# Optimization experiments

Measured on AMD Instinct MI355X. Metric: run time of the kernel, lower is better.

Reference implementation:

```python
import jax, jax.numpy as jnp
import numpy as np

# SMPL-H kintree parents for the first 22 joints (kintree_table[0][:22]); root parent is unused.
SMPL_PARENT = np.array([0, 0, 0, 0, 1, 2, 3, 4, 5, 6, 7, 8, 9, 9, 9, 12, 13, 14, 16, 17, 18, 19], dtype=np.int64)

EPS = 1e-12


def _sixd2matrot(d6):
    # d6: [..., 6] -> R: [..., 3, 3] (rows b1,b2,b3), pytorch3d rotation_6d_to_matrix convention
    a1, a2 = d6[..., :3], d6[..., 3:]
    b1 = a1 / jnp.maximum(jnp.linalg.norm(a1, axis=-1, keepdims=True), EPS)
    a2p = a2 - jnp.sum(b1 * a2, axis=-1, keepdims=True) * b1
    b2 = a2p / jnp.maximum(jnp.linalg.norm(a2p, axis=-1, keepdims=True), EPS)
    b3 = jnp.cross(b1, b2)
    return jnp.stack([b1, b2, b3], axis=-2)


def setup_inputs() -> dict:
    key = jax.random.key(0)
    B, T, J = 512, 196, 22
    pred_pose = jax.random.normal(key, (B, T, J * 6), dtype=jnp.float32)
    return {"pred_pose": pred_pose, "parent": SMPL_PARENT}


def reference(pred_pose, parent):
    B, T, C = pred_pose.shape  # C = 22*6
    J = C // 6
    parent = np.asarray(parent)  # static tree structure
    d6 = pred_pose.reshape(B * T, J, 6)
    R_local = _sixd2matrot(d6)  # [N, J, 3, 3]
    # forward kinematics along the tree: R_global[i] = R_global[parent[i]] @ R_local[i]
    R_global = [R_local[:, 0]]
    for i in range(1, J):
        R_global.append(jnp.einsum('nij,njk->nik', R_global[int(parent[i])], R_local[:, i]))
    R_global = jnp.stack(R_global, axis=1)  # [N, J, 3, 3]
    # matrot -> 6d: first two rows flattened
    rotation_global_r6d = R_global[..., :2, :].reshape(B, T, J * 6)
    return rotation_global_r6d
```

## Files before the change

kernel.cpp:

```cpp
#include <hip/hip_runtime.h>


#define TPB 256

namespace {
constexpr int PAR1[22] = {0,0,0,0,1,2,3,4,5,6,7,8,9,9,9,12,13,14,16,17,18,19};
constexpr int PAR2[22] = {0,0,0,0,0,0,0,1,2,3,4,5,6,6,6,9,9,9,13,14,16,17};
constexpr int PAR4[22] = {0,0,0,0,0,0,0,0,0,0,0,0,0,0,0,3,3,3,6,6,9,9};

__device__ __host__ constexpr unsigned long long pack5(const int (&t)[22], int base) {
    unsigned long long v = 0;
    for (int i = 0; i < 11; ++i)
        v |= (unsigned long long)(t[base + i] & 31) << (5 * i);
    return v;
}
constexpr unsigned long long P1L = pack5(PAR1, 0), P1H = pack5(PAR1, 11);
constexpr unsigned long long P2L = pack5(PAR2, 0), P2H = pack5(PAR2, 11);
constexpr unsigned long long P4L = pack5(PAR4, 0), P4H = pack5(PAR4, 11);
}

__device__ __forceinline__ void mm3(float* __restrict__ D, const float* __restrict__ P,
                                    const float* __restrict__ L) {
#pragma unroll
    for (int r = 0; r < 3; ++r)
#pragma unroll
        for (int c = 0; c < 3; ++c)
            D[3 * r + c] = P[3 * r + 0] * L[0 + c] +
                           P[3 * r + 1] * L[3 + c] +
                           P[3 * r + 2] * L[6 + c];
}

__global__ __launch_bounds__(TPB) void fk6d_kernel(const float* __restrict__ in,
                                                   float* __restrict__ out, int N)
{
    const int tid = threadIdx.x;
    const int lane = tid & 63;
    const int base = lane & 32;
    const int j = lane & 31;
    const int frame = blockIdx.x * 8 + ((tid >> 6) << 1) + (lane >> 5);
    const bool act = (j < 22) && (frame < N);
    const int jc = (j < 22) ? j : 21;
    const int jm = (jc < 11) ? jc : jc - 11;
    const int sh = 5 * jm;

    const int a1 = (int)(((jc < 11) ? P1L : P1H) >> sh) & 31;
    const int a2 = (int)(((jc < 11) ? P2L : P2H) >> sh) & 31;
    const int a4 = (int)(((jc < 11) ? P4L : P4H) >> sh) & 31;

    float A[9];
    if (act) {
        const float* s = in + (size_t)frame * 132 + j * 6;
        float2 d0 = *reinterpret_cast<const float2*>(s);
        float2 d1 = *reinterpret_cast<const float2*>(s + 2);
        float2 d2 = *reinterpret_cast<const float2*>(s + 4);
        float a1x = d0.x, a1y = d0.y, a1z = d1.x;
        float a2x = d1.y, a2y = d2.x, a2z = d2.y;
        float n1 = sqrtf(a1x * a1x + a1y * a1y + a1z * a1z);
        float i1 = 1.0f / fmaxf(n1, 1e-12f);
        float b1x = a1x * i1, b1y = a1y * i1, b1z = a1z * i1;
        float dt = b1x * a2x + b1y * a2y + b1z * a2z;
        float cx = a2x - dt * b1x, cy = a2y - dt * b1y, cz = a2z - dt * b1z;
        float n2 = sqrtf(cx * cx + cy * cy + cz * cz);
        float i2 = 1.0f / fmaxf(n2, 1e-12f);
        A[0] = b1x; A[1] = b1y; A[2] = b1z;
        A[3] = cx * i2; A[4] = cy * i2; A[5] = cz * i2;
        A[6] = A[1] * A[5] - A[2] * A[4];
        A[7] = A[2] * A[3] - A[0] * A[5];
        A[8] = A[0] * A[4] - A[1] * A[3];
    } else {
#pragma unroll
        for (int k = 0; k < 9; ++k) A[k] = 0.0f;
    }

    {
        float M[9], T[9];
        int src = base | a1;
#pragma unroll
        for (int k = 0; k < 9; ++k) M[k] = __shfl(A[k], src, 64);
        mm3(T, M, A);
        bool on = (j >= 1);
#pragma unroll
        for (int k = 0; k < 9; ++k) A[k] = on ? T[k] : A[k];
    }
    {
        float M[9], T[9];
        int src = base | a2;
#pragma unroll
        for (int k = 0; k < 9; ++k) M[k] = __shfl(A[k], src, 64);
        mm3(T, M, A);
        bool on = (j >= 4);
#pragma unroll
        for (int k = 0; k < 9; ++k) A[k] = on ? T[k] : A[k];
    }
    {
        float M[9], T[9];
        int src = base | a4;
#pragma unroll
        for (int k = 0; k < 9; ++k) M[k] = __shfl(A[k], src, 64);
        mm3(T, M, A);
        bool on = (j >= 10);
#pragma unroll
        for (int k = 0; k < 9; ++k) A[k] = on ? T[k] : A[k];
    }

    if (act) {
        float* d = out + (size_t)frame * 132 + j * 6;
        *reinterpret_cast<float2*>(d)     = make_float2(A[0], A[1]);
        *reinterpret_cast<float2*>(d + 2) = make_float2(A[2], A[3]);
        *reinterpret_cast<float2*>(d + 4) = make_float2(A[4], A[5]);
    }
}

extern "C" void kernel_launch(void* const* d_in, const int* in_sizes, int n_in,
                              void* d_out, int out_size, void* d_ws, size_t ws_size,
                              hipStream_t stream) {
    const float* in = (const float*)d_in[0];
    float* out = (float*)d_out;
    int N = in_sizes[0] / 132;
    int grid = (N + 7) / 8;
    fk6d_kernel<<<grid, TPB, 0, stream>>>(in, out, N);
}
```

Baseline: 28.75 us.

## Stage frame tiles through LDS with async global-to-LDS loads and coalesced stores

Each block now handles a 16-frame tile. The tile is loaded straight into shared memory with global_load_lds, which replaces the strided float2 global loads. Results are written back into LDS, then copied out to global memory as contiguous float4 stores. Block size doubles to 512 with a launch-bounds occupancy hint. A scalar tail kernel covers leftover frames, and it adds a barrier and LDS pressure per block.

```diff
diff --git a/kernel.cpp b/kernel.cpp
--- a/kernel.cpp
+++ b/kernel.cpp
@@ -1,7 +1,9 @@
 #include <hip/hip_runtime.h>
 
 
-#define TPB 256
+#define TPB 512
+#define TILE_FRAMES 16
+#define TILE_FLOATS (TILE_FRAMES * 132)
 
 namespace {
 constexpr int PAR1[22] = {0,0,0,0,1,2,3,4,5,6,7,8,9,9,9,12,13,14,16,17,18,19};
@@ -30,26 +32,43 @@
                            P[3 * r + 2] * L[6 + c];
 }
 
-__global__ __launch_bounds__(TPB) void fk6d_kernel(const float* __restrict__ in,
-                                                   float* __restrict__ out, int N)
+__global__ __launch_bounds__(TPB, 6) void fk6d_kernel(const float* __restrict__ in,
+                                                      float* __restrict__ out)
 {
+    __shared__ float lds[TILE_FLOATS];
     const int tid = threadIdx.x;
+    const int wid = tid >> 6;
     const int lane = tid & 63;
+
+    const float* gin = in + (size_t)blockIdx.x * TILE_FLOATS;
+    float* gout = out + (size_t)blockIdx.x * TILE_FLOATS;
+
+    __builtin_amdgcn_global_load_lds(
+        (const __attribute__((address_space(1))) void*)(gin + wid * 256 + lane * 4),
+        (__attribute__((address_space(3))) void*)(lds + wid * 256), 16, 0, 0);
+    if (wid == 0) {
+        __builtin_amdgcn_global_load_lds(
+            (const __attribute__((address_space(1))) void*)(gin + 2048 + lane),
+            (__attribute__((address_space(3))) void*)(lds + 2048), 4, 0, 0);
+    }
+    __syncthreads();
+
     const int base = lane & 32;
     const int j = lane & 31;
-    const int frame = blockIdx.x * 8 + ((tid >> 6) << 1) + (lane >> 5);
-    const bool act = (j < 22) && (frame < N);
-    const int jc = (j < 22) ? j : 21;
+    const int frame = wid * 2 + (lane >> 5);
+    const bool act = (j < 22);
+    const int jc = act ? j : 21;
     const int jm = (jc < 11) ? jc : jc - 11;
     const int sh = 5 * jm;
-
     const int a1 = (int)(((jc < 11) ? P1L : P1H) >> sh) & 31;
     const int a2 = (int)(((jc < 11) ? P2L : P2H) >> sh) & 31;
     const int a4 = (int)(((jc < 11) ? P4L : P4H) >> sh) & 31;
 
     float A[9];
+#pragma unroll
+    for (int k = 0; k < 9; ++k) A[k] = 0.0f;
     if (act) {
-        const float* s = in + (size_t)frame * 132 + j * 6;
+        const float* s = lds + frame * 132 + j * 6;
         float2 d0 = *reinterpret_cast<const float2*>(s);
         float2 d1 = *reinterpret_cast<const float2*>(s + 2);
         float2 d2 = *reinterpret_cast<const float2*>(s + 4);
@@ -67,9 +86,6 @@
         A[6] = A[1] * A[5] - A[2] * A[4];
         A[7] = A[2] * A[3] - A[0] * A[5];
         A[8] = A[0] * A[4] - A[1] * A[3];
-    } else {
-#pragma unroll
-        for (int k = 0; k < 9; ++k) A[k] = 0.0f;
     }
 
     {
@@ -104,10 +120,52 @@
     }
 
     if (act) {
-        float* d = out + (size_t)frame * 132 + j * 6;
+        float* d = lds + frame * 132 + j * 6;
         *reinterpret_cast<float2*>(d)     = make_float2(A[0], A[1]);
         *reinterpret_cast<float2*>(d + 2) = make_float2(A[2], A[3]);
         *reinterpret_cast<float2*>(d + 4) = make_float2(A[4], A[5]);
+    }
+    __syncthreads();
+
+    const float4* l4 = reinterpret_cast<const float4*>(lds);
+    float4* o4 = reinterpret_cast<float4*>(gout);
+#pragma unroll
+    for (int t = tid; t < TILE_FLOATS / 4; t += TPB) o4[t] = l4[t];
+}
+
+__global__ void fk6d_tail(const float* __restrict__ in, float* __restrict__ out,
+                          int n0, int N) {
+    constexpr int PAR[22] = {0, 0, 0, 0, 1, 2, 3, 4, 5, 6, 7, 8, 9, 9, 9,
+                             12, 13, 14, 16, 17, 18, 19};
+    int n = n0 + blockIdx.x * blockDim.x + threadIdx.x;
+    if (n >= N) return;
+    const float* src = in + (size_t)n * 132;
+    float* dst = out + (size_t)n * 132;
+    float Rg[22][9];
+#pragma unroll
+    for (int j = 0; j < 22; ++j) {
+        const float* s = src + 6 * j;
+        float Lr[9];
+        float n1 = sqrtf(s[0]*s[0] + s[1]*s[1] + s[2]*s[2]);
+        float i1 = 1.0f / fmaxf(n1, 1e-12f);
+        float b1x = s[0]*i1, b1y = s[1]*i1, b1z = s[2]*i1;
+        float dt = b1x*s[3] + b1y*s[4] + b1z*s[5];
+        float cx = s[3]-dt*b1x, cy = s[4]-dt*b1y, cz = s[5]-dt*b1z;
+        float n2 = sqrtf(cx*cx + cy*cy + cz*cz);
+        float i2 = 1.0f / fmaxf(n2, 1e-12f);
+        Lr[0]=b1x; Lr[1]=b1y; Lr[2]=b1z;
+        Lr[3]=cx*i2; Lr[4]=cy*i2; Lr[5]=cz*i2;
+        Lr[6]=Lr[1]*Lr[5]-Lr[2]*Lr[4];
+        Lr[7]=Lr[2]*Lr[3]-Lr[0]*Lr[5];
+        Lr[8]=Lr[0]*Lr[4]-Lr[1]*Lr[3];
+        if (j == 0) {
+#pragma unroll
+            for (int k = 0; k < 9; ++k) Rg[0][k] = Lr[k];
+        } else {
+            mm3(Rg[j], Rg[PAR[j]], Lr);
+        }
+#pragma unroll
+        for (int k = 0; k < 6; ++k) dst[6 * j + k] = Rg[j][k];
     }
 }
 
@@ -117,6 +175,9 @@
     const float* in = (const float*)d_in[0];
     float* out = (float*)d_out;
     int N = in_sizes[0] / 132;
-    int grid = (N + 7) / 8;
-    fk6d_kernel<<<grid, TPB, 0, stream>>>(in, out, N);
+    int NT = N / TILE_FRAMES;
+    if (NT > 0) fk6d_kernel<<<NT, TPB, 0, stream>>>(in, out);
+    int rem = N - NT * TILE_FRAMES;
+    if (rem > 0)
+        fk6d_tail<<<(rem + 63) / 64, 64, 0, stream>>>(in, out, NT * TILE_FRAMES, N);
 }
```

Measured after the change: 29.79 us. 1.04x slower.
